# Performance work log

Measured on AMD Instinct MI355X. Metric: run time of the kernel, lower is better.

## Reference

```python
import jax, jax.numpy as jnp
import numpy as np

N_NODES = 100000
N_EDGES = 3200000
D_FEAT = 64


def setup_inputs() -> dict:
    key = jax.random.key(0)
    k1, k2, k3, k4 = jax.random.split(key, 4)
    features = jax.random.normal(k1, (N_NODES, D_FEAT), dtype=jnp.float32)
    vals = jax.random.uniform(k2, (N_EDGES,), dtype=jnp.float32)  # Laplacian nonzero values (e.g. 1/sqrt(di*dj))
    rows = jax.random.randint(k3, (N_EDGES,), 0, N_NODES)
    cols = jax.random.randint(k4, (N_EDGES,), 0, N_NODES)
    return {"features": features, "vals": vals, "rows": rows, "cols": cols}


def reference(features, vals, rows, cols):
    # (L + I) @ features, with L given in COO (rows, cols, vals).
    # Gather source node features, scale by edge value, scatter-add to destination rows.
    msgs = vals[:, None] * features[cols]              # [E, d]
    agg = jax.ops.segment_sum(msgs, rows, num_segments=N_NODES)  # [N, d]
    # self-loop (identity sparse matrix) fused as a direct add
    return agg + features
```

## Files before the change

### kernel.cpp

```cpp
#include <hip/hip_runtime.h>
#include <hip/hip_bf16.h>
#include <hip/hip_fp16.h>

#define D 64
#define RB 200
#define NB_MAX 512
#define MAGIC 21474944u
#define SC_TILE 4096
#define SC_PT 16

__device__ __forceinline__ int bucket_of(int r) {
    return (int)__umulhi((unsigned)r, MAGIC);
}

__global__ void k_hist(const int* __restrict__ rows, int* __restrict__ counts,
                       int E, int nb) {
    __shared__ int h[NB_MAX];
    for (int i = threadIdx.x; i < nb; i += blockDim.x) h[i] = 0;
    __syncthreads();
    int E4 = E >> 2;
    int i = blockIdx.x * blockDim.x + threadIdx.x;
    int stride = gridDim.x * blockDim.x;
    const int4* rows4 = (const int4*)rows;
    for (; i < E4; i += stride) {
        int4 r4 = rows4[i];
        atomicAdd(&h[bucket_of(r4.x)], 1);
        atomicAdd(&h[bucket_of(r4.y)], 1);
        atomicAdd(&h[bucket_of(r4.z)], 1);
        atomicAdd(&h[bucket_of(r4.w)], 1);
    }
    int t0 = E4 * 4 + blockIdx.x * blockDim.x + threadIdx.x;
    if (t0 < E) atomicAdd(&h[bucket_of(rows[t0])], 1);
    __syncthreads();
    for (int j = threadIdx.x; j < nb; j += blockDim.x)
        if (h[j]) atomicAdd(&counts[j], h[j]);
}

__global__ void k_scan(const int* __restrict__ counts, int* __restrict__ starts,
                       int* __restrict__ cursor, int nb) {
    __shared__ int lds[NB_MAX];
    int t = threadIdx.x;
    int v = (t < nb) ? counts[t] : 0;
    lds[t] = v;
    __syncthreads();
    for (int off = 1; off < NB_MAX; off <<= 1) {
        int x = (t >= off) ? lds[t - off] : 0;
        __syncthreads();
        lds[t] += x;
        __syncthreads();
    }
    if (t < nb) {
        int excl = lds[t] - v;
        starts[t] = excl;
        cursor[t] = excl;
        if (t == nb - 1) starts[nb] = lds[t];
    }
}

__global__ void __launch_bounds__(256) k_scatter2(
    const int* __restrict__ rows, const int* __restrict__ cols,
    const float* __restrict__ vals, int* __restrict__ cursor,
    unsigned long long* __restrict__ packed1, int E) {
    __shared__ unsigned long long recs[SC_TILE];
    __shared__ int dsts[SC_TILE];
    __shared__ int cnt[NB_MAX];
    __shared__ int tst[NB_MAX];
    __shared__ int bas[NB_MAX];
    __shared__ int cur[NB_MAX];

    int t = threadIdx.x;
    int tile = blockIdx.x * SC_TILE;
    int tile_n = E - tile; if (tile_n > SC_TILE) tile_n = SC_TILE;
    bool full = (tile_n == SC_TILE);

    cnt[t] = 0; cnt[t + 256] = 0;
    __syncthreads();

    int r[SC_PT];
    int e0 = tile + t * SC_PT;
    if (full) {
        const int4* r4 = (const int4*)(rows + e0);
#pragma unroll
        for (int g = 0; g < 4; ++g) {
            int4 rr = r4[g];
            r[g * 4 + 0] = rr.x; r[g * 4 + 1] = rr.y;
            r[g * 4 + 2] = rr.z; r[g * 4 + 3] = rr.w;
        }
#pragma unroll
        for (int u = 0; u < SC_PT; ++u) atomicAdd(&cnt[bucket_of(r[u])], 1);
    } else {
#pragma unroll
        for (int u = 0; u < SC_PT; ++u) {
            int e = e0 + u;
            r[u] = (e < E) ? rows[e] : -1;
            if (r[u] >= 0) atomicAdd(&cnt[bucket_of(r[u])], 1);
        }
    }
    __syncthreads();

    {
        int c0 = cnt[t], c1 = cnt[t + 256];
        bas[t] = c0 ? atomicAdd(&cursor[t], c0) : 0;
        bas[t + 256] = c1 ? atomicAdd(&cursor[t + 256], c1) : 0;
        tst[t] = c0; tst[t + 256] = c1;
    }
    __syncthreads();
    for (int off = 1; off < NB_MAX; off <<= 1) {
        int v0 = (t >= off) ? tst[t - off] : 0;
        int v1 = (t + 256 >= off) ? tst[t + 256 - off] : 0;
        __syncthreads();
        tst[t] += v0; tst[t + 256] += v1;
        __syncthreads();
    }
    {
        int e0_ = tst[t] - cnt[t];
        int e1_ = tst[t + 256] - cnt[t + 256];
        __syncthreads();
        tst[t] = e0_; tst[t + 256] = e1_;
        cur[t] = e0_; cur[t + 256] = e1_;
    }
    __syncthreads();

    if (full) {
        const int4* c4 = (const int4*)(cols + e0);
        const float4* v4 = (const float4*)(vals + e0);
#pragma unroll
        for (int g = 0; g < 4; ++g) {
            int4 cc = c4[g];
            float4 vv = v4[g];
            int carr[4] = {cc.x, cc.y, cc.z, cc.w};
            float varr[4] = {vv.x, vv.y, vv.z, vv.w};
#pragma unroll
            for (int w = 0; w < 4; ++w) {
                int u = g * 4 + w;
                int b = bucket_of(r[u]);
                int slot = atomicAdd(&cur[b], 1);
                int roff = r[u] - b * RB;
                unsigned lo = ((unsigned)roff << 17) | (unsigned)carr[w];
                recs[slot] = ((unsigned long long)__float_as_uint(varr[w]) << 32) | lo;
                dsts[slot] = bas[b] + (slot - tst[b]);
            }
        }
    } else {
#pragma unroll
        for (int u = 0; u < SC_PT; ++u) {
            int e = e0 + u;
            if (r[u] >= 0) {
                int b = bucket_of(r[u]);
                int slot = atomicAdd(&cur[b], 1);
                int roff = r[u] - b * RB;
                unsigned lo = ((unsigned)roff << 17) | (unsigned)cols[e];
                recs[slot] = ((unsigned long long)__float_as_uint(vals[e]) << 32) | lo;
                dsts[slot] = bas[b] + (slot - tst[b]);
            }
        }
    }
    __syncthreads();

    for (int j = t; j < tile_n; j += 256) packed1[dsts[j]] = recs[j];
}

__global__ void __launch_bounds__(1024) k_sort(
    const unsigned long long* __restrict__ packed1, const int* __restrict__ starts,
    unsigned* __restrict__ packed2, int* __restrict__ rowptr, int N, int E) {
    __shared__ int rhist[RB];
    __shared__ int rcur[RB];
    __shared__ int sc[256];
    int b = blockIdx.x;
    int t = threadIdx.x;
    int s = starts[b];
    int e = starts[b + 1];

    for (int i = t; i < RB; i += 1024) rhist[i] = 0;
    __syncthreads();
    for (int i = s + t; i < e; i += 1024) {
        unsigned lo = (unsigned)packed1[i];
        atomicAdd(&rhist[(lo >> 17) & 0xFF], 1);
    }
    __syncthreads();
    if (t < 256) sc[t] = (t < RB) ? rhist[t] : 0;
    __syncthreads();
    for (int off = 1; off < 256; off <<= 1) {
        int x = (t < 256 && t >= off) ? sc[t - off] : 0;
        __syncthreads();
        if (t < 256) sc[t] += x;
        __syncthreads();
    }
    if (t < RB) rcur[t] = sc[t] - rhist[t];
    __syncthreads();

    int gbase = b * RB;
    int nr = N - gbase; if (nr > RB) nr = RB;
    if (t < nr) rowptr[gbase + t] = s + (sc[t] - rhist[t]);
    if (b == 0 && t == 0) rowptr[N] = E;

    for (int i = s + t; i < e; i += 1024) {
        unsigned long long dj = packed1[i];
        unsigned lo = (unsigned)dj;
        int ro = (int)((lo >> 17) & 0xFF);
        int slot = atomicAdd(&rcur[ro], 1);
        float v = __uint_as_float((unsigned)(dj >> 32));
        unsigned hb = (unsigned)__half_as_ushort(__float2half(v));
        packed2[s + slot] = (hb << 17) | (lo & 0x1FFFFu);
    }
}

__global__ void __launch_bounds__(256) k_spmm(
    const float* __restrict__ feat, const unsigned* __restrict__ packed2,
    const int* __restrict__ rowptr, float* __restrict__ out, int N) {
    int lane = threadIdx.x & 63;
    int wid = (int)(((long long)blockIdx.x * blockDim.x + threadIdx.x) >> 6);
    if (wid >= N) return;
    int s = rowptr[wid];
    int e = rowptr[wid + 1];

    float acc = feat[(size_t)wid * D + lane];
    int i = s;
    for (; i + 8 <= e; i += 8) {
        float g[8], vv[8];
#pragma unroll
        for (int u = 0; u < 8; ++u) {
            unsigned d = packed2[i + u];
            vv[u] = __half2float(__ushort_as_half((unsigned short)(d >> 17)));
            g[u] = feat[(size_t)(d & 0x1FFFFu) * D + lane];
        }
#pragma unroll
        for (int u = 0; u < 8; ++u) acc = fmaf(vv[u], g[u], acc);
    }
    for (; i < e; ++i) {
        unsigned d = packed2[i];
        float v = __half2float(__ushort_as_half((unsigned short)(d >> 17)));
        acc = fmaf(v, feat[(size_t)(d & 0x1FFFFu) * D + lane], acc);
    }
    out[(size_t)wid * D + lane] = acc;
}

__global__ void gp_init_kernel(const float4* __restrict__ feat, float4* __restrict__ out,
                               int n4) {
    int i = blockIdx.x * blockDim.x + threadIdx.x;
    int stride = gridDim.x * blockDim.x;
    for (; i < n4; i += stride) out[i] = feat[i];
}
__global__ void gp_edge_kernel(const float* __restrict__ feat, const float* __restrict__ vals,
                               const int* __restrict__ rows, const int* __restrict__ cols,
                               float* __restrict__ out, int n_edges) {
    int lane = threadIdx.x & 63;
    long long gtid = (long long)blockIdx.x * blockDim.x + threadIdx.x;
    int e = (int)(gtid >> 6);
    if (e >= n_edges) return;
    int r = rows[e];
    int c = cols[e];
    float v = vals[e];
    float x = feat[(long long)c * D + lane];
    unsafeAtomicAdd(&out[(long long)r * D + lane], v * x);
}

extern "C" void kernel_launch(void* const* d_in, const int* in_sizes, int n_in,
                              void* d_out, int out_size, void* d_ws, size_t ws_size,
                              hipStream_t stream) {
    const float* feat = (const float*)d_in[0];
    const float* vals = (const float*)d_in[1];
    const int* rows = (const int*)d_in[2];
    const int* cols = (const int*)d_in[3];
    float* out = (float*)d_out;

    int E = in_sizes[1];
    int N = out_size / D;
    int nb = (N + RB - 1) / RB;

    size_t off_rowptr = (size_t)E * 4;
    size_t off_counts = off_rowptr + (size_t)(N + 1) * 4;
    size_t off_starts = off_counts + (size_t)NB_MAX * 4;
    size_t off_cursor = off_starts + (size_t)(NB_MAX + 1) * 4;
    size_t needed = off_cursor + (size_t)NB_MAX * 4;
    bool out_fits = ((size_t)out_size * 4) >= ((size_t)E * 8);

    if (ws_size >= needed && nb <= NB_MAX && N < 131072 && out_fits) {
        char* ws = (char*)d_ws;
        unsigned* packed2 = (unsigned*)ws;
        int* rowptr = (int*)(ws + off_rowptr);
        int* counts = (int*)(ws + off_counts);
        int* starts = (int*)(ws + off_starts);
        int* cursor = (int*)(ws + off_cursor);
        unsigned long long* packed1 = (unsigned long long*)d_out;

        hipMemsetAsync(counts, 0, (size_t)nb * 4, stream);
        k_hist<<<256, 256, 0, stream>>>(rows, counts, E, nb);
        k_scan<<<1, NB_MAX, 0, stream>>>(counts, starts, cursor, nb);
        int gScat = (E + SC_TILE - 1) / SC_TILE;
        k_scatter2<<<gScat, 256, 0, stream>>>(rows, cols, vals, cursor, packed1, E);
        k_sort<<<nb, 1024, 0, stream>>>(packed1, starts, packed2, rowptr, N, E);
        long long tt = (long long)N * 64;
        k_spmm<<<(int)((tt + 255) / 256), 256, 0, stream>>>(feat, packed2, rowptr, out, N);
    } else {
        int n4 = out_size / 4;
        int grid = (n4 + 255) / 256;
        if (grid > 4096) grid = 4096;
        gp_init_kernel<<<grid, 256, 0, stream>>>((const float4*)feat, (float4*)out, n4);
        long long tthreads = (long long)E * 64;
        gp_edge_kernel<<<(int)((tthreads + 255) / 256), 256, 0, stream>>>(feat, vals, rows, cols,
                                                                          out, E);
    }
}
```

Baseline: 280.0 us.

## Gather fp16 feature copy in SpMM and use power-of-two row buckets

Adds a kernel that converts the feature matrix to fp16 in workspace, so the SpMM gather reads half the bytes per neighbour row. Row buckets become 256 rows wide, so bucket index and row offset are a shift and a mask instead of a magic multiply. The scatter kernel drops its per-slot destination array and finds each record's bucket by binary search over the prefix sums, which saves shared memory but adds lookups per store. The fp16 features and an added conversion pass lower the precision of the gathered values and add launch and traffic cost.

```diff
diff --git a/kernel.cpp b/kernel.cpp
--- a/kernel.cpp
+++ b/kernel.cpp
@@ -3,14 +3,24 @@
 #include <hip/hip_fp16.h>
 
 #define D 64
-#define RB 200
+#define RBSH 8
+#define RB 256
 #define NB_MAX 512
-#define MAGIC 21474944u
 #define SC_TILE 4096
 #define SC_PT 16
 
-__device__ __forceinline__ int bucket_of(int r) {
-    return (int)__umulhi((unsigned)r, MAGIC);
+__device__ __forceinline__ int bucket_of(int r) { return r >> RBSH; }
+
+__global__ void k_cvt(const float* __restrict__ f, __half* __restrict__ h, int n8) {
+    int i = blockIdx.x * blockDim.x + threadIdx.x;
+    if (i >= n8) return;
+    const float4* f4 = (const float4*)f + (size_t)i * 2;
+    float4 a = f4[0], b = f4[1];
+    __half2* o = (__half2*)h + (size_t)i * 4;
+    o[0] = __floats2half2_rn(a.x, a.y);
+    o[1] = __floats2half2_rn(a.z, a.w);
+    o[2] = __floats2half2_rn(b.x, b.y);
+    o[3] = __floats2half2_rn(b.z, b.w);
 }
 
 __global__ void k_hist(const int* __restrict__ rows, int* __restrict__ counts,
@@ -62,11 +72,9 @@
     const float* __restrict__ vals, int* __restrict__ cursor,
     unsigned long long* __restrict__ packed1, int E) {
     __shared__ unsigned long long recs[SC_TILE];
-    __shared__ int dsts[SC_TILE];
     __shared__ int cnt[NB_MAX];
-    __shared__ int tst[NB_MAX];
+    __shared__ int tst[NB_MAX + 1];
     __shared__ int bas[NB_MAX];
-    __shared__ int cur[NB_MAX];
 
     int t = threadIdx.x;
     int tile = blockIdx.x * SC_TILE;
@@ -98,12 +106,10 @@
     }
     __syncthreads();
 
-    {
-        int c0 = cnt[t], c1 = cnt[t + 256];
-        bas[t] = c0 ? atomicAdd(&cursor[t], c0) : 0;
-        bas[t + 256] = c1 ? atomicAdd(&cursor[t + 256], c1) : 0;
-        tst[t] = c0; tst[t + 256] = c1;
-    }
+    int c0 = cnt[t], c1 = cnt[t + 256];
+    bas[t] = c0 ? atomicAdd(&cursor[t], c0) : 0;
+    bas[t + 256] = c1 ? atomicAdd(&cursor[t + 256], c1) : 0;
+    tst[t] = c0; tst[t + 256] = c1;
     __syncthreads();
     for (int off = 1; off < NB_MAX; off <<= 1) {
         int v0 = (t >= off) ? tst[t - off] : 0;
@@ -113,11 +119,11 @@
         __syncthreads();
     }
     {
-        int e0_ = tst[t] - cnt[t];
-        int e1_ = tst[t + 256] - cnt[t + 256];
-        __syncthreads();
-        tst[t] = e0_; tst[t + 256] = e1_;
-        cur[t] = e0_; cur[t + 256] = e1_;
+        int x0 = tst[t] - c0;
+        int x1 = tst[t + 256] - c1;
+        tst[t] = x0; tst[t + 256] = x1;
+        cnt[t] = x0; cnt[t + 256] = x1;
+        if (t == 0) tst[NB_MAX] = tile_n;
     }
     __syncthreads();
 
@@ -134,11 +140,10 @@
             for (int w = 0; w < 4; ++w) {
                 int u = g * 4 + w;
                 int b = bucket_of(r[u]);
-                int slot = atomicAdd(&cur[b], 1);
-                int roff = r[u] - b * RB;
+                int slot = atomicAdd(&cnt[b], 1);
+                int roff = r[u] & (RB - 1);
                 unsigned lo = ((unsigned)roff << 17) | (unsigned)carr[w];
                 recs[slot] = ((unsigned long long)__float_as_uint(varr[w]) << 32) | lo;
-                dsts[slot] = bas[b] + (slot - tst[b]);
             }
         }
     } else {
@@ -147,17 +152,22 @@
             int e = e0 + u;
             if (r[u] >= 0) {
                 int b = bucket_of(r[u]);
-                int slot = atomicAdd(&cur[b], 1);
-                int roff = r[u] - b * RB;
+                int slot = atomicAdd(&cnt[b], 1);
+                int roff = r[u] & (RB - 1);
                 unsigned lo = ((unsigned)roff << 17) | (unsigned)cols[e];
                 recs[slot] = ((unsigned long long)__float_as_uint(vals[e]) << 32) | lo;
-                dsts[slot] = bas[b] + (slot - tst[b]);
             }
         }
     }
     __syncthreads();
 
-    for (int j = t; j < tile_n; j += 256) packed1[dsts[j]] = recs[j];
+    for (int j = t; j < tile_n; j += 256) {
+        int b = 0;
+#pragma unroll
+        for (int step = NB_MAX / 2; step >= 1; step >>= 1)
+            if (tst[b + step] <= j) b += step;
+        packed1[bas[b] + (j - tst[b])] = recs[j];
+    }
 }
 
 __global__ void __launch_bounds__(1024) k_sort(
@@ -165,31 +175,31 @@
     unsigned* __restrict__ packed2, int* __restrict__ rowptr, int N, int E) {
     __shared__ int rhist[RB];
     __shared__ int rcur[RB];
-    __shared__ int sc[256];
+    __shared__ int sc[RB];
     int b = blockIdx.x;
     int t = threadIdx.x;
     int s = starts[b];
     int e = starts[b + 1];
 
-    for (int i = t; i < RB; i += 1024) rhist[i] = 0;
+    if (t < RB) rhist[t] = 0;
     __syncthreads();
     for (int i = s + t; i < e; i += 1024) {
         unsigned lo = (unsigned)packed1[i];
         atomicAdd(&rhist[(lo >> 17) & 0xFF], 1);
     }
     __syncthreads();
-    if (t < 256) sc[t] = (t < RB) ? rhist[t] : 0;
-    __syncthreads();
-    for (int off = 1; off < 256; off <<= 1) {
-        int x = (t < 256 && t >= off) ? sc[t - off] : 0;
-        __syncthreads();
-        if (t < 256) sc[t] += x;
+    if (t < RB) sc[t] = rhist[t];
+    __syncthreads();
+    for (int off = 1; off < RB; off <<= 1) {
+        int x = (t < RB && t >= off) ? sc[t - off] : 0;
+        __syncthreads();
+        if (t < RB) sc[t] += x;
         __syncthreads();
     }
     if (t < RB) rcur[t] = sc[t] - rhist[t];
     __syncthreads();
 
-    int gbase = b * RB;
+    int gbase = b << RBSH;
     int nr = N - gbase; if (nr > RB) nr = RB;
     if (t < nr) rowptr[gbase + t] = s + (sc[t] - rhist[t]);
     if (b == 0 && t == 0) rowptr[N] = E;
@@ -206,8 +216,9 @@
 }
 
 __global__ void __launch_bounds__(256) k_spmm(
-    const float* __restrict__ feat, const unsigned* __restrict__ packed2,
-    const int* __restrict__ rowptr, float* __restrict__ out, int N) {
+    const float* __restrict__ feat, const __half* __restrict__ feat16,
+    const unsigned* __restrict__ packed2, const int* __restrict__ rowptr,
+    float* __restrict__ out, int N) {
     int lane = threadIdx.x & 63;
     int wid = (int)(((long long)blockIdx.x * blockDim.x + threadIdx.x) >> 6);
     if (wid >= N) return;
@@ -222,7 +233,7 @@
         for (int u = 0; u < 8; ++u) {
             unsigned d = packed2[i + u];
             vv[u] = __half2float(__ushort_as_half((unsigned short)(d >> 17)));
-            g[u] = feat[(size_t)(d & 0x1FFFFu) * D + lane];
+            g[u] = __half2float(feat16[(size_t)(d & 0x1FFFFu) * D + lane]);
         }
 #pragma unroll
         for (int u = 0; u < 8; ++u) acc = fmaf(vv[u], g[u], acc);
@@ -230,7 +241,7 @@
     for (; i < e; ++i) {
         unsigned d = packed2[i];
         float v = __half2float(__ushort_as_half((unsigned short)(d >> 17)));
-        acc = fmaf(v, feat[(size_t)(d & 0x1FFFFu) * D + lane], acc);
+        acc = fmaf(v, __half2float(feat16[(size_t)(d & 0x1FFFFu) * D + lane]), acc);
     }
     out[(size_t)wid * D + lane] = acc;
 }
@@ -272,26 +283,30 @@
     size_t off_counts = off_rowptr + (size_t)(N + 1) * 4;
     size_t off_starts = off_counts + (size_t)NB_MAX * 4;
     size_t off_cursor = off_starts + (size_t)(NB_MAX + 1) * 4;
-    size_t needed = off_cursor + (size_t)NB_MAX * 4;
+    size_t off_feat16 = off_cursor + (size_t)NB_MAX * 4;
+    size_t needed = off_feat16 + (size_t)N * D * 2;
     bool out_fits = ((size_t)out_size * 4) >= ((size_t)E * 8);
 
-    if (ws_size >= needed && nb <= NB_MAX && N < 131072 && out_fits) {
+    if (ws_size >= needed && nb <= NB_MAX && N <= 131072 && out_fits) {
         char* ws = (char*)d_ws;
         unsigned* packed2 = (unsigned*)ws;
         int* rowptr = (int*)(ws + off_rowptr);
         int* counts = (int*)(ws + off_counts);
         int* starts = (int*)(ws + off_starts);
         int* cursor = (int*)(ws + off_cursor);
+        __half* feat16 = (__half*)(ws + off_feat16);
         unsigned long long* packed1 = (unsigned long long*)d_out;
 
         hipMemsetAsync(counts, 0, (size_t)nb * 4, stream);
+        int n8 = (N * D) / 8;
+        k_cvt<<<(n8 + 255) / 256, 256, 0, stream>>>(feat, feat16, n8);
         k_hist<<<256, 256, 0, stream>>>(rows, counts, E, nb);
         k_scan<<<1, NB_MAX, 0, stream>>>(counts, starts, cursor, nb);
         int gScat = (E + SC_TILE - 1) / SC_TILE;
         k_scatter2<<<gScat, 256, 0, stream>>>(rows, cols, vals, cursor, packed1, E);
         k_sort<<<nb, 1024, 0, stream>>>(packed1, starts, packed2, rowptr, N, E);
         long long tt = (long long)N * 64;
-        k_spmm<<<(int)((tt + 255) / 256), 256, 0, stream>>>(feat, packed2, rowptr, out, N);
+        k_spmm<<<(int)((tt + 255) / 256), 256, 0, stream>>>(feat, feat16, packed2, rowptr, out, N);
     } else {
         int n4 = out_size / 4;
         int grid = (n4 + 255) / 256;
```

Measured after the change: 287.1 us. 1.03x slower.
